# Kernel tuning notes

Measured on AMD Instinct MI355X. Metric: run time of the kernel, lower is better.

The kernel has to match this reference:

```python
import jax, jax.numpy as jnp
import numpy as np

# Cleaned/faithful JAX port of TATLMPLayer. The original torch code has obvious
# typos (edge_type_feature_embedding used before assignment, self.weight_mlp vs
# self._weight_mlp, missing dim= in concatenate, elementwise mult of (B,E,K) with
# (K,D)); we implement the clearly intended math: two-level masked-softmax
# message passing over an incidence matrix H, gumbel-softmax typed edge
# embeddings, and a 4-head cross-attention to polyline features.

NEG_SLOPE = 0.01  # torch leaky_relu default
TAU = 0.5         # gumbel-softmax temperature 1/2


def _mlp(x, W1, b1, W2, b2):
    return jnp.maximum(x @ W1 + b1, 0.0) @ W2 + b2


def setup_inputs() -> dict:
    B, N, E, P, D, T, K, Hd = 2, 256, 512, 256, 128, 8, 8, 256
    key = jax.random.key(0)
    ks = jax.random.split(key, 40)
    g = lambda i, shape, s=0.05: jax.random.normal(ks[i], shape, dtype=jnp.float32) * s
    return {
        "agent_features": jax.random.normal(ks[0], (B, N, D), dtype=jnp.float32),
        "agent_types": jax.random.uniform(ks[1], (B, N, T), dtype=jnp.float32),
        "polyline_features": jax.random.normal(ks[2], (B, P, D), dtype=jnp.float32),
        "H": (jax.random.uniform(ks[3], (B, E, N)) < 0.1).astype(jnp.float32),
        "type_emb": g(4, (K, D)),
        "w_W1": g(5, (2 * D, Hd)), "w_b1": g(6, (Hd,)), "w_W2": g(7, (Hd, 1)), "w_b2": g(8, (1,)),
        "d_W1": g(9, (D + T, Hd)), "d_b1": g(10, (Hd,)), "d_W2": g(11, (Hd, K)), "d_b2": g(12, (K,)),
        "f_W1": g(13, (D + T, Hd)), "f_b1": g(14, (Hd,)), "f_W2": g(15, (Hd, 1)), "f_b2": g(16, (1,)),
        "o_W1": g(17, (4 * D, Hd)), "o_b1": g(18, (Hd,)), "o_W2": g(19, (Hd, D)), "o_b2": g(20, (D,)),
        "q_W": g(21, (3 * D, D)), "q_b": g(22, (D,)),
        "k_W": g(23, (D, D)), "k_b": g(24, (D,)),
        "v_W": g(25, (D, D)), "v_b": g(26, (D,)),
        "iq_W": g(27, (D, D)), "iq_b": g(28, (D,)),
        "ik_W": g(29, (D, D)), "ik_b": g(30, (D,)),
        "iv_W": g(31, (D, D)), "iv_b": g(32, (D,)),
        "op_W": g(33, (D, D)), "op_b": g(34, (D,)),
    }


def reference(agent_features, agent_types, polyline_features, H, type_emb,
              w_W1, w_b1, w_W2, w_b2, d_W1, d_b1, d_W2, d_b2,
              f_W1, f_b1, f_W2, f_b2, o_W1, o_b1, o_W2, o_b2,
              q_W, q_b, k_W, k_b, v_W, v_b,
              iq_W, iq_b, ik_W, ik_b, iv_W, iv_b, op_W, op_b):
    B, N, D = agent_features.shape
    E = H.shape[1]

    # level 1: incidence-aggregated edge features
    ef_init = jnp.einsum('ben,bnd->bed', H, agent_features)            # (B,E,D)
    pair = jnp.concatenate([
        jnp.broadcast_to(ef_init[:, :, None, :], (B, E, N, D)),
        jnp.broadcast_to(agent_features[:, None, :, :], (B, E, N, D))], axis=-1)
    ew = _mlp(pair, w_W1, w_b1, w_W2, w_b2)[..., 0]                    # (B,E,N)
    Hw = jax.nn.softmax(ew * H, axis=2) * H
    edge_features = jnp.einsum('ben,bnd->bed', Hw, agent_features)     # (B,E,D)

    # typed edge embedding via gumbel-softmax over edge types
    edge_type = jnp.einsum('ben,bnt->bet', H, agent_types)             # (B,E,T)
    et = jnp.concatenate([edge_features, edge_type], axis=-1)          # (B,E,D+T)
    logits = _mlp(et, d_W1, d_b1, d_W2, d_b2)                          # (B,E,K)
    u = jax.random.uniform(jax.random.key(42), logits.shape, minval=1e-6, maxval=1.0 - 1e-6)
    gumbel = -jnp.log(-jnp.log(u))
    distribution = jax.nn.softmax((logits + gumbel) / TAU, axis=-1)
    factor = jax.nn.sigmoid(_mlp(et, f_W1, f_b1, f_W2, f_b2))          # (B,E,1)
    edge_type_embedding = jnp.einsum('bek,kd->bed', factor * distribution, type_emb)

    # level 2: masked edge->agent message passing
    pair2 = jnp.concatenate([
        jnp.broadcast_to(edge_type_embedding[:, :, None, :], (B, E, N, D)),
        jnp.broadcast_to(agent_features[:, None, :, :], (B, E, N, D))], axis=-1)
    pair2 = pair2 * H[..., None]
    hw2 = jnp.where(_mlp(pair2, w_W1, w_b1, w_W2, w_b2)[..., 0] > 0,
                    _mlp(pair2, w_W1, w_b1, w_W2, w_b2)[..., 0], 0.0)
    # leaky relu (single-eval form)
    raw2 = _mlp(pair2, w_W1, w_b1, w_W2, w_b2)[..., 0]
    hw2 = jnp.where(raw2 > 0, raw2, NEG_SLOPE * raw2)                  # (B,E,N)
    Hw2 = jax.nn.softmax(hw2, axis=2) * H
    msg = jnp.einsum('ben,bef->bnf', Hw2,
                     jnp.concatenate([edge_features, edge_type_embedding], axis=-1))
    agent_feat = jnp.concatenate([msg, agent_features], axis=-1)       # (B,N,3D)

    # cross-attention to polylines (4 heads)
    Q = agent_feat @ q_W + q_b
    Kp = polyline_features @ k_W + k_b
    Vp = polyline_features @ v_W + v_b
    q2 = Q @ iq_W + iq_b
    k2 = Kp @ ik_W + ik_b
    v2 = Vp @ iv_W + iv_b
    nh, hd = 4, D // 4
    qh = q2.reshape(B, N, nh, hd)
    kh = k2.reshape(B, -1, nh, hd)
    vh = v2.reshape(B, -1, nh, hd)
    att = jax.nn.softmax(jnp.einsum('bqhd,bkhd->bhqk', qh, kh) / jnp.sqrt(jnp.float32(hd)), axis=-1)
    o = jnp.einsum('bhqk,bkhd->bqhd', att, vh).reshape(B, N, D)
    polyline_new = o @ op_W + op_b                                     # (B,N,D)

    agent_new = _mlp(jnp.concatenate([agent_feat, polyline_new], axis=-1),
                     o_W1, o_b1, o_W2, o_b2)                           # (B,N,D)
    return agent_new, polyline_new
```

## Files before the change

### kernel.cpp

```cpp
#include <hip/hip_runtime.h>
#include <math.h>

#define BB 2
#define NN 256
#define EE 512
#define PP 256
#define DD 128
#define TT 8
#define KK 8
#define HDIM 256

#define WS_G      0
#define WS_C0     8192
#define WS_V      8256
#define WS_EDGEF  139328
#define WS_ETE    270400
#define WS_HWT    401472
#define WS_K2     663616
#define WS_V2     729152

#define PB_GUM 16
#define PB_V   272
#define PB_END 528

__device__ inline unsigned rotl32(unsigned x, int d){ return (x<<d)|(x>>(32-d)); }

__device__ inline float bits_to_gumbel(unsigned bits){
  float f = __uint_as_float((bits>>9)|0x3f800000u) - 1.0f;
  const float minv = 1e-6f;
  const float maxv = 1.0f - 1e-6f;
  float u = f*(maxv-minv) + minv;
  u = fmaxf(minv, u);
  return -logf(-logf(u));
}

__device__ __forceinline__ void f4fma(float4& a, float x, const float4& w){
  a.x += x*w.x; a.y += x*w.y; a.z += x*w.z; a.w += x*w.w;
}

__device__ __forceinline__ void block_reduce2_sum(float v[2], float* wred){
  int lane = threadIdx.x & 63, wid = threadIdx.x >> 6;
  #pragma unroll
  for (int s=32;s>0;s>>=1){
    #pragma unroll
    for (int r=0;r<2;r++){ v[r] += __shfl_xor(v[r], s, 64); }
  }
  if (lane==0){
    #pragma unroll
    for (int r=0;r<2;r++) wred[wid*2+r]=v[r];
  }
  __syncthreads();
  #pragma unroll
  for (int r=0;r<2;r++)
    v[r] = (wred[0*2+r]+wred[1*2+r]) + (wred[2*2+r]+wred[3*2+r]);
  __syncthreads();
}

__device__ __forceinline__ void mlp128_lds2(const float (*in)[DD], const float* W, const float* bias,
                                            float (*outl)[DD], float* part, int t){
  int c=(t&31)*4, ks=t>>5;
  float4 a[2];
  #pragma unroll
  for (int r=0;r<2;r++) a[r]=make_float4(0.f,0.f,0.f,0.f);
  #pragma unroll 4
  for (int i=ks*16;i<ks*16+16;i++){
    float4 w = *(const float4*)&W[(size_t)i*DD+c];
    #pragma unroll
    for (int r=0;r<2;r++) f4fma(a[r], in[r][i], w);
  }
  #pragma unroll
  for (int r=0;r<2;r++) *(float4*)&part[(ks*2+r)*DD+c]=a[r];
  __syncthreads();
  int cc=t&127, r=t>>7;
  {
    float s=0.f;
    #pragma unroll
    for (int k2=0;k2<8;k2++) s+=part[(k2*2+r)*DD+cc];
    outl[r][cc]=s+bias[cc];
  }
  __syncthreads();
}

__device__ __forceinline__ void mlp128_glob2(const float (*in)[DD], const float* W, const float* bias,
                                             float* dst, int r0, float* part, int t){
  int c=(t&31)*4, ks=t>>5;
  float4 a[2];
  #pragma unroll
  for (int r=0;r<2;r++) a[r]=make_float4(0.f,0.f,0.f,0.f);
  #pragma unroll 4
  for (int i=ks*16;i<ks*16+16;i++){
    float4 w = *(const float4*)&W[(size_t)i*DD+c];
    #pragma unroll
    for (int r=0;r<2;r++) f4fma(a[r], in[r][i], w);
  }
  #pragma unroll
  for (int r=0;r<2;r++) *(float4*)&part[(ks*2+r)*DD+c]=a[r];
  __syncthreads();
  int cc=t&127, r=t>>7;
  {
    float s=0.f;
    #pragma unroll
    for (int k2=0;k2<8;k2++) s+=part[(k2*2+r)*DD+cc];
    dst[(size_t)(r0+r)*DD+cc]=s+bias[cc];
  }
  __syncthreads();
}

__global__ void prep_kernel(float* g, float* c0, const float* w_b1,
                            const float* w_W2, const float* w_b2,
                            const float* af, const float* wW1, float* Vout,
                            const float* pf,
                            const float* kW, const float* kb, const float* ikW, const float* ikb,
                            const float* vW, const float* vb, const float* ivW, const float* ivb,
                            float* k2, float* v2){
  __shared__ float xs[2][DD];
  __shared__ float part[2048];
  __shared__ float wred[16];
  __shared__ float bufB[2][DD];
  int blk = blockIdx.x;
  int t = threadIdx.x;

  if (blk < PB_GUM){
    int j = blk*256 + t;
    {
      const unsigned k0=0u, k1=42u;
      const unsigned ks2 = k0^k1^0x1BD11BDAu;
      unsigned x0 = (unsigned)j, x1 = (unsigned)j + 4096u;
      const int r0_[4]={13,15,26,6}, r1_[4]={17,29,16,24};
      x0 += k0; x1 += k1;
      #pragma unroll
      for(int i=0;i<4;i++){ x0+=x1; x1=rotl32(x1,r0_[i]); x1^=x0; }
      x0+=k1; x1+=ks2+1u;
      #pragma unroll
      for(int i=0;i<4;i++){ x0+=x1; x1=rotl32(x1,r1_[i]); x1^=x0; }
      x0+=ks2; x1+=k0+2u;
      #pragma unroll
      for(int i=0;i<4;i++){ x0+=x1; x1=rotl32(x1,r0_[i]); x1^=x0; }
      x0+=k0; x1+=k1+3u;
      #pragma unroll
      for(int i=0;i<4;i++){ x0+=x1; x1=rotl32(x1,r1_[i]); x1^=x0; }
      x0+=k1; x1+=ks2+4u;
      #pragma unroll
      for(int i=0;i<4;i++){ x0+=x1; x1=rotl32(x1,r0_[i]); x1^=x0; }
      x0+=ks2; x1+=k0+5u;
      g[j]      = bits_to_gumbel(x0);
      g[j+4096] = bits_to_gumbel(x1);
    }
    if (blk == 0){
      float v4[2];
      v4[0] = fmaxf(w_b1[t],0.f)*w_W2[t]; v4[1]=0.f;
      block_reduce2_sum(v4, wred);
      if (t==0) c0[0] = v4[0] + w_b2[0];
    }
  } else if (blk < PB_V){
    int r0 = (blk - PB_GUM)*2;
    const float* W = wW1 + (size_t)DD*HDIM;
    for (int i=t;i<2*DD;i+=256) xs[i>>7][i&127] = af[(size_t)(r0+(i>>7))*DD + (i&127)];
    __syncthreads();
    int c = (t&63)*4, ks = t>>6;
    float4 acc[2];
    #pragma unroll
    for (int r=0;r<2;r++) acc[r]=make_float4(0.f,0.f,0.f,0.f);
    #pragma unroll 8
    for (int i=ks*32; i<ks*32+32; i++){
      float4 w = *(const float4*)&W[(size_t)i*HDIM + c];
      #pragma unroll
      for (int r=0;r<2;r++) f4fma(acc[r], xs[r][i], w);
    }
    #pragma unroll
    for (int r=0;r<2;r++) *(float4*)&part[(ks*2+r)*HDIM + c] = acc[r];
    __syncthreads();
    #pragma unroll
    for (int r=0;r<2;r++){
      float s = (part[(0*2+r)*HDIM+t] + part[(1*2+r)*HDIM+t])
              + (part[(2*2+r)*HDIM+t] + part[(3*2+r)*HDIM+t]);
      Vout[(size_t)(r0+r)*HDIM + t] = s;
    }
  } else {
    int r0 = (blk - PB_V)*2;
    for (int i=t;i<2*DD;i+=256) xs[i>>7][i&127] = pf[(size_t)(r0+(i>>7))*DD + (i&127)];
    __syncthreads();
    mlp128_lds2 (xs, kW, kb, bufB, part, t);
    mlp128_glob2(bufB, ikW, ikb, k2, r0, part, t);
    mlp128_lds2 (xs, vW, vb, bufB, part, t);
    mlp128_glob2(bufB, ivW, ivb, v2, r0, part, t);
  }
}

__global__ __launch_bounds__(512) void edge_kernel(
                            const float* Hm, const float* af, const float* at,
                            const float* Vm,
                            const float* wW1, const float* wb1, const float* wW2, const float* wb2,
                            const float* dW1, const float* db1, const float* dW2, const float* db2,
                            const float* fW1, const float* fb1, const float* fW2, const float* fb2,
                            const float* type_emb, const float* g, const float* c0p,
                            float* edgef_g, float* ete_g, float* HwT){
  __shared__ float bufA[8192];
  __shared__ float w2s[HDIM*KK];
  __shared__ float w2l[HDIM];
  __shared__ float et4[4][144];
  __shared__ float hd4[4][HDIM];
  __shared__ float redsm[512];
  __shared__ float wred[16];
  __shared__ float mred[4], sinv[4];
  __shared__ float facs[4];
  __shared__ float zz[4][KK];
  __shared__ float pzs[4][KK];
  __shared__ float fdv[4][KK];
  __shared__ int   hcnt[4];
  __shared__ int   hcomp[4*256];

  int e0 = blockIdx.x*4;
  int b  = e0 >> 9;
  int t  = threadIdx.x;
  int lane = t & 63, wid = t >> 6;

  if (t < HDIM) w2l[t] = wW2[t];
  for (int i=t;i<HDIM*KK;i+=512) w2s[i] = dW2[i];

  if (wid < 4){
    int r = wid;
    const float* Hrow = Hm + (size_t)(e0+r)*NN;
    int base = 0;
    #pragma unroll
    for (int c4=0;c4<4;c4++){
      int n2 = c4*64 + lane;
      bool pred = (Hrow[n2] != 0.f);
      unsigned long long mask = __ballot(pred);
      int off = __popcll(mask & ((1ull<<lane)-1ull));
      if (pred) hcomp[r*256+base+off] = n2;
      base += __popcll(mask);
    }
    if (lane==0) hcnt[r] = base;
  }
  __syncthreads();
  {
    int d = t & 127, r = t >> 7;
    int tot = hcnt[r];
    float a = 0.f, a2 = 0.f;
    for (int i=0;i<tot;i++){
      int n2 = hcomp[r*256+i];
      a += af[((size_t)b*NN+n2)*DD + d];
      if (d < TT) a2 += at[((size_t)b*NN+n2)*TT + d];
    }
    et4[r][d] = a;
    if (d < TT) et4[r][DD+d] = a2;
  }
  __syncthreads();
  {
    int c=(t&63)*4, ks=t>>6;
    float4 acc[4];
    #pragma unroll
    for (int r=0;r<4;r++) acc[r]=make_float4(0.f,0.f,0.f,0.f);
    #pragma unroll 4
    for (int i=ks*16; i<ks*16+16; i++){
      float4 w = *(const float4*)&wW1[(size_t)i*HDIM + c];
      #pragma unroll
      for (int r=0;r<4;r++) f4fma(acc[r], et4[r][i], w);
    }
    #pragma unroll
    for (int r=0;r<4;r++) *(float4*)&bufA[(ks*4+r)*HDIM + c] = acc[r];
  }
  __syncthreads();
  {
    int h=t&255, rh=t>>8;
    float bv = wb1[h];
    #pragma unroll
    for (int rr=0;rr<2;rr++){
      int r = 2*rh+rr;
      float s=0.f;
      #pragma unroll
      for (int k=0;k<8;k++) s += bufA[(k*4+r)*HDIM + h];
      hd4[r][h] = s + bv;
    }
  }
  __syncthreads();
  {
    int n = t&255, hh = t>>8;
    const float4* Vrow = (const float4*)(Vm + ((size_t)(b*NN)+n)*HDIM);
    float acc[4]={0.f,0.f,0.f,0.f};
    #pragma unroll 4
    for (int ii=hh*32; ii<hh*32+32; ii++){
      float4 v = Vrow[ii];
      float w0=w2l[4*ii+0], w1=w2l[4*ii+1], wc=w2l[4*ii+2], w3=w2l[4*ii+3];
      #pragma unroll
      for (int r=0;r<4;r++){
        acc[r] += fmaxf(hd4[r][4*ii+0]+v.x,0.f)*w0
                + fmaxf(hd4[r][4*ii+1]+v.y,0.f)*w1
                + fmaxf(hd4[r][4*ii+2]+v.z,0.f)*wc
                + fmaxf(hd4[r][4*ii+3]+v.w,0.f)*w3;
      }
    }
    #pragma unroll
    for (int r=0;r<4;r++) bufA[(hh*4+r)*256 + n] = acc[r];
  }
  __syncthreads();
  {
    int n = t&255, rh = t>>8;
    float b2v = wb2[0];
    #pragma unroll
    for (int rr=0;rr<2;rr++){
      int r = 2*rh+rr;
      float hv = Hm[(size_t)(e0+r)*NN + n];
      float xv = (hv!=0.f) ? (bufA[(0*4+r)*256+n] + bufA[(1*4+r)*256+n] + b2v) : 0.f;
      bufA[2048 + r*256 + n] = xv;
    }
  }
  __syncthreads();
  if (wid < 4){
    int r = wid;
    float v0=bufA[2048+r*256+lane],     v1=bufA[2048+r*256+lane+64],
          v2=bufA[2048+r*256+lane+128], v3=bufA[2048+r*256+lane+192];
    float m = fmaxf(fmaxf(v0,v1), fmaxf(v2,v3));
    #pragma unroll
    for (int s2=32;s2>0;s2>>=1) m = fmaxf(m, __shfl_xor(m, s2, 64));
    float ss = (expf(v0-m)+expf(v1-m)) + (expf(v2-m)+expf(v3-m));
    #pragma unroll
    for (int s2=32;s2>0;s2>>=1) ss += __shfl_xor(ss, s2, 64);
    if (lane==0){ mred[r]=m; sinv[r]=1.f/ss; }
  }
  __syncthreads();
  {
    int n = t&255, rh = t>>8;
    #pragma unroll
    for (int rr=0;rr<2;rr++){
      int r = 2*rh+rr;
      float hv = Hm[(size_t)(e0+r)*NN + n];
      float p = expf(bufA[2048+r*256+n] - mred[r]) * sinv[r];
      bufA[3072 + r*256 + n] = (hv!=0.f) ? p : 0.f;
    }
  }
  __syncthreads();
  {
    int d = t & 127, r = t >> 7;
    int tot = hcnt[r];
    float a = 0.f;
    for (int i=0;i<tot;i++){
      int n2 = hcomp[r*256+i];
      a += bufA[3072 + r*256 + n2] * af[((size_t)b*NN+n2)*DD + d];
    }
    et4[r][d] = a;
    edgef_g[(size_t)(e0+r)*DD + d] = a;
  }
  __syncthreads();
  {
    int half = t>>8, tt = t&255;
    int c=(tt&63)*4, ks=tt>>6;
    const float* W = half ? fW1 : dW1;
    float4 acc[4];
    #pragma unroll
    for (int r=0;r<4;r++) acc[r]=make_float4(0.f,0.f,0.f,0.f);
    #pragma unroll 4
    for (int i=ks*34;i<ks*34+34;i++){
      float4 w = *(const float4*)&W[(size_t)i*HDIM+c];
      #pragma unroll
      for (int r=0;r<4;r++) f4fma(acc[r], et4[r][i], w);
    }
    #pragma unroll
    for (int r=0;r<4;r++) *(float4*)&bufA[half*4096 + (ks*4+r)*HDIM + c] = acc[r];
  }
  __syncthreads();
  {
    int h=t&255, rh=t>>8;
    float bd = db1[h], bf = fb1[h], fw = fW2[h];
    float val[2];
    #pragma unroll
    for (int rr=0;rr<2;rr++){
      int r = 2*rh+rr;
      float sd=0.f, sf=0.f;
      #pragma unroll
      for (int k=0;k<4;k++){ sd += bufA[(k*4+r)*HDIM+h]; sf += bufA[4096+(k*4+r)*HDIM+h]; }
      hd4[r][h] = fmaxf(sd+bd, 0.f);
      val[rr] = fmaxf(sf+bf, 0.f)*fw;
    }
    #pragma unroll
    for (int s2=32;s2>0;s2>>=1){
      val[0] += __shfl_xor(val[0], s2, 64);
      val[1] += __shfl_xor(val[1], s2, 64);
    }
    if (lane==0){ wred[wid*2]=val[0]; wred[wid*2+1]=val[1]; }
  }
  __syncthreads();
  if (t<4){
    int r=t;
    int base = (r>=2)?4:0, off = r&1;
    float s = 0.f;
    #pragma unroll
    for (int w=0;w<4;w++) s += wred[(base+w)*2 + off];
    facs[r] = 1.f/(1.f+expf(-(s+fb2[0])));
  }
  __syncthreads();
  {
    int r_ = t>>7, rem = t&127, k_ = rem&7, j_ = rem>>3;
    float lp = 0.f;
    #pragma unroll 4
    for (int i=0;i<16;i++){
      int h = j_ + 16*i;
      lp += hd4[r_][h]*w2s[h*KK + k_];
    }
    redsm[t] = lp;
  }
  __syncthreads();
  if (t < 32){
    int r = t>>3, k = t&7;
    float s = db2[k] + g[(size_t)(e0+r)*KK + k];
    #pragma unroll
    for (int j=0;j<16;j++) s += redsm[r*128 + j*8 + k];
    zz[r][k] = s*2.0f;
  }
  __syncthreads();
  if (t < 32){
    int r = t>>3, k = t&7;
    float m = zz[r][0];
    #pragma unroll
    for (int k2=1;k2<KK;k2++) m = fmaxf(m, zz[r][k2]);
    pzs[r][k] = expf(zz[r][k]-m);
  }
  __syncthreads();
  if (t < 32){
    int r = t>>3, k = t&7;
    float s = 0.f;
    #pragma unroll
    for (int k2=0;k2<KK;k2++) s += pzs[r][k2];
    fdv[r][k] = facs[r]*pzs[r][k]/s;
  }
  __syncthreads();
  {
    int d = t&127, r = t>>7;
    float a = 0.f;
    #pragma unroll
    for (int k=0;k<KK;k++) a += fdv[r][k]*type_emb[(size_t)k*DD + d];
    et4[r][d] = a;
    ete_g[(size_t)(e0+r)*DD + d] = a;
  }
  __syncthreads();
  {
    int c=(t&63)*4, ks=t>>6;
    float4 acc[4];
    #pragma unroll
    for (int r=0;r<4;r++) acc[r]=make_float4(0.f,0.f,0.f,0.f);
    #pragma unroll 4
    for (int i=ks*16; i<ks*16+16; i++){
      float4 w = *(const float4*)&wW1[(size_t)i*HDIM + c];
      #pragma unroll
      for (int r=0;r<4;r++) f4fma(acc[r], et4[r][i], w);
    }
    #pragma unroll
    for (int r=0;r<4;r++) *(float4*)&bufA[(ks*4+r)*HDIM + c] = acc[r];
  }
  __syncthreads();
  {
    int h=t&255, rh=t>>8;
    float bv = wb1[h];
    #pragma unroll
    for (int rr=0;rr<2;rr++){
      int r = 2*rh+rr;
      float s=0.f;
      #pragma unroll
      for (int k=0;k<8;k++) s += bufA[(k*4+r)*HDIM + h];
      hd4[r][h] = s + bv;
    }
  }
  __syncthreads();
  {
    int n = t&255, hh = t>>8;
    const float4* Vrow = (const float4*)(Vm + ((size_t)(b*NN)+n)*HDIM);
    float acc[4]={0.f,0.f,0.f,0.f};
    #pragma unroll 4
    for (int ii=hh*32; ii<hh*32+32; ii++){
      float4 v = Vrow[ii];
      float w0=w2l[4*ii+0], w1=w2l[4*ii+1], wc=w2l[4*ii+2], w3=w2l[4*ii+3];
      #pragma unroll
      for (int r=0;r<4;r++){
        acc[r] += fmaxf(hd4[r][4*ii+0]+v.x,0.f)*w0
                + fmaxf(hd4[r][4*ii+1]+v.y,0.f)*w1
                + fmaxf(hd4[r][4*ii+2]+v.z,0.f)*wc
                + fmaxf(hd4[r][4*ii+3]+v.w,0.f)*w3;
      }
    }
    #pragma unroll
    for (int r=0;r<4;r++) bufA[(hh*4+r)*256 + n] = acc[r];
  }
  __syncthreads();
  {
    int n = t&255, rh = t>>8;
    float b2v = wb2[0];
    float c0 = c0p[0];
    #pragma unroll
    for (int rr=0;rr<2;rr++){
      int r = 2*rh+rr;
      float hv = Hm[(size_t)(e0+r)*NN + n];
      float raw = (hv!=0.f) ? (bufA[(0*4+r)*256+n] + bufA[(1*4+r)*256+n] + b2v) : c0;
      bufA[2048 + r*256 + n] = raw>0.f ? raw : 0.01f*raw;
    }
  }
  __syncthreads();
  if (wid < 4){
    int r = wid;
    float v0=bufA[2048+r*256+lane],     v1=bufA[2048+r*256+lane+64],
          v2=bufA[2048+r*256+lane+128], v3=bufA[2048+r*256+lane+192];
    float m = fmaxf(fmaxf(v0,v1), fmaxf(v2,v3));
    #pragma unroll
    for (int s2=32;s2>0;s2>>=1) m = fmaxf(m, __shfl_xor(m, s2, 64));
    float ss = (expf(v0-m)+expf(v1-m)) + (expf(v2-m)+expf(v3-m));
    #pragma unroll
    for (int s2=32;s2>0;s2>>=1) ss += __shfl_xor(ss, s2, 64);
    if (lane==0){ mred[r]=m; sinv[r]=1.f/ss; }
  }
  __syncthreads();
  if (t < 256){
    int n = t;
    float o[4];
    #pragma unroll
    for (int r=0;r<4;r++){
      float hv = Hm[(size_t)(e0+r)*NN + n];
      float p = expf(bufA[2048+r*256+n] - mred[r]) * sinv[r];
      o[r] = (hv!=0.f) ? p : 0.f;
    }
    int eb = e0 & 511;
    float4 o4; o4.x=o[0]; o4.y=o[1]; o4.z=o[2]; o4.w=o[3];
    *(float4*)(HwT + ((size_t)(b*NN)+n)*EE + eb) = o4;
  }
}

__global__ void agent_kernel(const float* HwT, const float* edgef, const float* ete,
                             const float* af,
                             const float* qW, const float* qb, const float* iqW, const float* iqb,
                             const float* k2, const float* v2,
                             const float* op_W, const float* op_b,
                             const float* oW1, const float* ob1,
                             const float* oW2, const float* ob2,
                             float* pnew, float* anew){
  __shared__ int   ecomp[EE];
  __shared__ float wcomp[EE];
  __shared__ int   wcnt[4];
  __shared__ float agfl[512];
  __shared__ float part[1024];
  __shared__ float Qs[DD];
  __shared__ float qr[DD];
  __shared__ float att[4][PP+1];
  __shared__ float o_l[DD];
  __shared__ float hid[HDIM];
  int bn = blockIdx.x; int b = bn >> 8; int t = threadIdx.x;
  int lane = t & 63, wid = t >> 6;

  {
    const float* wrow = HwT + (size_t)bn*EE;
    int total = 0;
    #pragma unroll
    for (int p=0;p<2;p++){
      int e = p*256 + t;
      float w = wrow[e];
      bool pred = (w != 0.f);
      unsigned long long mask = __ballot(pred);
      if (lane==0) wcnt[wid] = __popcll(mask);
      int off = __popcll(mask & ((1ull<<lane)-1ull));
      __syncthreads();
      int wb = total;
      for (int ww=0; ww<wid; ww++) wb += wcnt[ww];
      if (pred){ ecomp[wb+off] = e; wcomp[wb+off] = w; }
      total += wcnt[0]+wcnt[1]+wcnt[2]+wcnt[3];
      __syncthreads();
    }
    float acc = 0.f;
    const float* srcbase = (t < DD) ? (edgef + (size_t)b*EE*DD + t)
                                    : (ete   + (size_t)b*EE*DD + (t-DD));
    for (int i=0;i<total;i++){
      acc += wcomp[i] * srcbase[(size_t)ecomp[i]*DD];
    }
    agfl[t] = acc;
    if (t < DD) agfl[2*DD+t] = af[(size_t)bn*DD + t];
  }
  __syncthreads();
  int c=(t&31)*4, ps=t>>5;
  {
    float4 a = make_float4(0.f,0.f,0.f,0.f);
    #pragma unroll 4
    for (int i=ps*48;i<ps*48+48;i++){
      float4 w = *(const float4*)&qW[(size_t)i*DD+c];
      f4fma(a, agfl[i], w);
    }
    *(float4*)&part[ps*DD+c]=a;
  }
  __syncthreads();
  if (t<DD){
    float s=0.f;
    #pragma unroll
    for (int k=0;k<8;k++) s+=part[k*DD+t];
    Qs[t]=s+qb[t];
  }
  __syncthreads();
  {
    float4 a = make_float4(0.f,0.f,0.f,0.f);
    #pragma unroll 4
    for (int i=ps*16;i<ps*16+16;i++){
      float4 w = *(const float4*)&iqW[(size_t)i*DD+c];
      f4fma(a, Qs[i], w);
    }
    *(float4*)&part[ps*DD+c]=a;
  }
  __syncthreads();
  if (t<DD){
    float s=0.f;
    #pragma unroll
    for (int k=0;k<8;k++) s+=part[k*DD+t];
    qr[t]=s+iqb[t];
  }
  __syncthreads();
  const float scale = 0.17677669529663687f;
  const float* krow = k2 + ((size_t)(b*PP) + t)*DD;
  #pragma unroll
  for (int h=0;h<4;h++){
    const float4* k4 = (const float4*)(krow + h*32);
    float s = 0.f;
    #pragma unroll
    for (int jj=0;jj<8;jj++){
      float4 kk = k4[jj];
      s += qr[h*32+jj*4+0]*kk.x + qr[h*32+jj*4+1]*kk.y
         + qr[h*32+jj*4+2]*kk.z + qr[h*32+jj*4+3]*kk.w;
    }
    att[h][t] = s*scale;
  }
  __syncthreads();
  {
    int h = wid;
    float v0 = att[h][lane],     v1 = att[h][lane+64],
          ve = att[h][lane+128], v3 = att[h][lane+192];
    float m = fmaxf(fmaxf(v0,v1), fmaxf(ve,v3));
    #pragma unroll
    for (int s2=32;s2>0;s2>>=1) m = fmaxf(m, __shfl_xor(m, s2, 64));
    float e0 = expf(v0-m), e1 = expf(v1-m), e2 = expf(ve-m), e3 = expf(v3-m);
    float ss = (e0+e1)+(e2+e3);
    #pragma unroll
    for (int s2=32;s2>0;s2>>=1) ss += __shfl_xor(ss, s2, 64);
    float inv = 1.f/ss;
    att[h][lane] = e0*inv; att[h][lane+64] = e1*inv;
    att[h][lane+128] = e2*inv; att[h][lane+192] = e3*inv;
  }
  __syncthreads();
  int h2 = c >> 5;
  {
    float4 acc = make_float4(0.f,0.f,0.f,0.f);
    #pragma unroll 4
    for (int i=0;i<32;i++){
      int p = ps*32+i;
      float4 v = *(const float4*)&v2[((size_t)(b*PP)+p)*DD + c];
      f4fma(acc, att[h2][p], v);
    }
    *(float4*)&part[ps*DD+c]=acc;
  }
  __syncthreads();
  if (t<DD){
    float s=0.f;
    #pragma unroll
    for (int k=0;k<8;k++) s+=part[k*DD+t];
    o_l[t]=s;
  }
  __syncthreads();
  {
    float4 a2 = make_float4(0.f,0.f,0.f,0.f);
    #pragma unroll 4
    for (int i=ps*16;i<ps*16+16;i++){
      float4 w = *(const float4*)&op_W[(size_t)i*DD + c];
      f4fma(a2, o_l[i], w);
    }
    *(float4*)&part[ps*DD+c]=a2;
  }
  __syncthreads();
  if (t<DD){
    float s=0.f;
    #pragma unroll
    for (int k=0;k<8;k++) s+=part[k*DD+t];
    float pv = s+op_b[t];
    agfl[3*DD+t] = pv;
    pnew[(size_t)bn*DD+t] = pv;
  }
  __syncthreads();
  {
    int c1=(t&63)*4, ks1=t>>6;
    float4 acc = make_float4(0.f,0.f,0.f,0.f);
    #pragma unroll 8
    for (int i=ks1*128;i<ks1*128+128;i++){
      float4 w = *(const float4*)&oW1[(size_t)i*HDIM+c1];
      f4fma(acc, agfl[i], w);
    }
    *(float4*)&part[ks1*HDIM+c1]=acc;
  }
  __syncthreads();
  {
    float s = (part[0*HDIM+t]+part[1*HDIM+t]) + (part[2*HDIM+t]+part[3*HDIM+t]);
    hid[t] = fmaxf(s+ob1[t], 0.f);
  }
  __syncthreads();
  {
    float4 a2 = make_float4(0.f,0.f,0.f,0.f);
    #pragma unroll 8
    for (int h=ps*32;h<ps*32+32;h++){
      float4 w = *(const float4*)&oW2[(size_t)h*DD+c];
      f4fma(a2, hid[h], w);
    }
    *(float4*)&part[ps*DD+c]=a2;
  }
  __syncthreads();
  if (t<DD){
    float s=0.f;
    #pragma unroll
    for (int k=0;k<8;k++) s+=part[k*DD+t];
    anew[(size_t)bn*DD+t]=s+ob2[t];
  }
}

extern "C" void kernel_launch(void* const* d_in, const int* in_sizes, int n_in,
                              void* d_out, int out_size, void* d_ws, size_t ws_size,
                              hipStream_t stream) {
  const float* af       = (const float*)d_in[0];
  const float* at       = (const float*)d_in[1];
  const float* pf       = (const float*)d_in[2];
  const float* Hm       = (const float*)d_in[3];
  const float* type_emb = (const float*)d_in[4];
  const float* w_W1 = (const float*)d_in[5];
  const float* w_b1 = (const float*)d_in[6];
  const float* w_W2 = (const float*)d_in[7];
  const float* w_b2 = (const float*)d_in[8];
  const float* d_W1 = (const float*)d_in[9];
  const float* d_b1 = (const float*)d_in[10];
  const float* d_W2 = (const float*)d_in[11];
  const float* d_b2 = (const float*)d_in[12];
  const float* f_W1 = (const float*)d_in[13];
  const float* f_b1 = (const float*)d_in[14];
  const float* f_W2 = (const float*)d_in[15];
  const float* f_b2 = (const float*)d_in[16];
  const float* o_W1 = (const float*)d_in[17];
  const float* o_b1 = (const float*)d_in[18];
  const float* o_W2 = (const float*)d_in[19];
  const float* o_b2 = (const float*)d_in[20];
  const float* q_W  = (const float*)d_in[21];
  const float* q_b  = (const float*)d_in[22];
  const float* k_W  = (const float*)d_in[23];
  const float* k_b  = (const float*)d_in[24];
  const float* v_W  = (const float*)d_in[25];
  const float* v_b  = (const float*)d_in[26];
  const float* iq_W = (const float*)d_in[27];
  const float* iq_b = (const float*)d_in[28];
  const float* ik_W = (const float*)d_in[29];
  const float* ik_b = (const float*)d_in[30];
  const float* iv_W = (const float*)d_in[31];
  const float* iv_b = (const float*)d_in[32];
  const float* op_W = (const float*)d_in[33];
  const float* op_b = (const float*)d_in[34];

  float* ws   = (float*)d_ws;
  float* out  = (float*)d_out;
  float* anew = out;
  float* pnew = out + BB*NN*DD;

  prep_kernel<<<PB_END, 256, 0, stream>>>(
      ws+WS_G, ws+WS_C0, w_b1, w_W2, w_b2,
      af, w_W1, ws+WS_V,
      pf, k_W,k_b,ik_W,ik_b, v_W,v_b,iv_W,iv_b,
      ws+WS_K2, ws+WS_V2);
  edge_kernel<<<256,512,0,stream>>>(
      Hm, af, at, ws+WS_V,
      w_W1, w_b1, w_W2, w_b2,
      d_W1,d_b1,d_W2,d_b2, f_W1,f_b1,f_W2,f_b2,
      type_emb, ws+WS_G, ws+WS_C0,
      ws+WS_EDGEF, ws+WS_ETE, ws+WS_HWT);
  agent_kernel<<<BB*NN,256,0,stream>>>(
      ws+WS_HWT, ws+WS_EDGEF, ws+WS_ETE, af,
      q_W, q_b, iq_W, iq_b,
      ws+WS_K2, ws+WS_V2, op_W, op_b,
      o_W1,o_b1,o_W2,o_b2, pnew, anew);
}
```

Before: 90.60 us.

## Move edge first-layer precompute into prep kernel and process two agents per block

The incidence gather and first MLP layer for edges (edge-sum features, type sums, hidden layer U1) move from the edge kernel into extra blocks of the prep kernel, so that work runs in parallel with the other prep blocks. The edge kernel now preloads its w_W1 slice into registers for the later second-level matmul. The agent kernel handles two agents per 512-thread block, so each weight load serves two rows. This adds workspace traffic and register pressure (16 float4 per thread in the edge kernel), which could lower occupancy.

```diff
diff --git a/kernel.cpp b/kernel.cpp
--- a/kernel.cpp
+++ b/kernel.cpp
@@ -13,15 +13,18 @@
 #define WS_G      0
 #define WS_C0     8192
 #define WS_V      8256
-#define WS_EDGEF  139328
-#define WS_ETE    270400
-#define WS_HWT    401472
-#define WS_K2     663616
-#define WS_V2     729152
+#define WS_U1     139328
+#define WS_ETYPE  401472
+#define WS_EDGEF  409664
+#define WS_ETE    540736
+#define WS_HWT    671808
+#define WS_K2     933952
+#define WS_V2     999488
 
 #define PB_GUM 16
-#define PB_V   272
-#define PB_END 528
+#define PB_INC 272
+#define PB_V   528
+#define PB_END 784
 
 __device__ inline unsigned rotl32(unsigned x, int d){ return (x<<d)|(x>>(32-d)); }
 
@@ -108,17 +111,23 @@
 
 __global__ void prep_kernel(float* g, float* c0, const float* w_b1,
                             const float* w_W2, const float* w_b2,
-                            const float* af, const float* wW1, float* Vout,
+                            const float* Hm, const float* af, const float* at,
+                            const float* wW1, const float* wb1,
+                            float* U1g, float* etype_g, float* Vout,
                             const float* pf,
                             const float* kW, const float* kb, const float* ikW, const float* ikb,
                             const float* vW, const float* vb, const float* ivW, const float* ivb,
                             float* k2, float* v2){
+  __shared__ float part[4096];
+  __shared__ float wred[16];
+  __shared__ int   hcomp[4*256];
+  __shared__ int   hcnt[4];
+  __shared__ float ef[4][DD];
   __shared__ float xs[2][DD];
-  __shared__ float part[2048];
-  __shared__ float wred[16];
   __shared__ float bufB[2][DD];
   int blk = blockIdx.x;
   int t = threadIdx.x;
+  int lane = t & 63, wid = t >> 6;
 
   if (blk < PB_GUM){
     int j = blk*256 + t;
@@ -152,8 +161,68 @@
       block_reduce2_sum(v4, wred);
       if (t==0) c0[0] = v4[0] + w_b2[0];
     }
+  } else if (blk < PB_INC){
+    int e0 = (blk - PB_GUM)*4;
+    int b = e0 >> 9;
+    {
+      int r = wid;
+      const float* Hrow = Hm + (size_t)(e0+r)*NN;
+      int base = 0;
+      #pragma unroll
+      for (int c4=0;c4<4;c4++){
+        int n2 = c4*64 + lane;
+        bool pred = (Hrow[n2] != 0.f);
+        unsigned long long mask = __ballot(pred);
+        int off = __popcll(mask & ((1ull<<lane)-1ull));
+        if (pred) hcomp[r*256+base+off] = n2;
+        base += __popcll(mask);
+      }
+      if (lane==0) hcnt[r] = base;
+    }
+    __syncthreads();
+    {
+      int d = t & 127, eh = t >> 7;
+      #pragma unroll
+      for (int rr=0;rr<2;rr++){
+        int r = eh*2 + rr;
+        int tot = hcnt[r];
+        float a = 0.f, a2 = 0.f;
+        for (int i=0;i<tot;i++){
+          int n2 = hcomp[r*256+i];
+          a += af[((size_t)b*NN+n2)*DD + d];
+          if (d < TT) a2 += at[((size_t)b*NN+n2)*TT + d];
+        }
+        ef[r][d] = a;
+        if (d < TT) etype_g[(size_t)(e0+r)*TT + d] = a2;
+      }
+    }
+    __syncthreads();
+    {
+      int c = (t&63)*4, ks = t>>6;
+      float4 acc[4];
+      #pragma unroll
+      for (int r=0;r<4;r++) acc[r]=make_float4(0.f,0.f,0.f,0.f);
+      #pragma unroll 8
+      for (int i=ks*32; i<ks*32+32; i++){
+        float4 w = *(const float4*)&wW1[(size_t)i*HDIM + c];
+        #pragma unroll
+        for (int r=0;r<4;r++) f4fma(acc[r], ef[r][i], w);
+      }
+      #pragma unroll
+      for (int r=0;r<4;r++) *(float4*)&part[(ks*4+r)*HDIM + c] = acc[r];
+    }
+    __syncthreads();
+    {
+      float bv = wb1[t];
+      #pragma unroll
+      for (int r=0;r<4;r++){
+        float s = (part[(0*4+r)*HDIM+t] + part[(1*4+r)*HDIM+t])
+                + (part[(2*4+r)*HDIM+t] + part[(3*4+r)*HDIM+t]);
+        U1g[(size_t)(e0+r)*HDIM + t] = s + bv;
+      }
+    }
   } else if (blk < PB_V){
-    int r0 = (blk - PB_GUM)*2;
+    int r0 = (blk - PB_INC)*2;
     const float* W = wW1 + (size_t)DD*HDIM;
     for (int i=t;i<2*DD;i+=256) xs[i>>7][i&127] = af[(size_t)(r0+(i>>7))*DD + (i&127)];
     __syncthreads();
@@ -188,8 +257,8 @@
 }
 
 __global__ __launch_bounds__(512) void edge_kernel(
-                            const float* Hm, const float* af, const float* at,
-                            const float* Vm,
+                            const float* Hm, const float* af,
+                            const float* Vm, const float* U1g, const float* etype_g,
                             const float* wW1, const float* wb1, const float* wW2, const float* wb2,
                             const float* dW1, const float* db1, const float* dW2, const float* db2,
                             const float* fW1, const float* fb1, const float* fW2, const float* fb2,
@@ -215,9 +284,23 @@
   int t  = threadIdx.x;
   int lane = t & 63, wid = t >> 6;
 
+  int cW=(t&63)*4, ksW=t>>6;
+  float4 wreg[16];
+  #pragma unroll
+  for (int i=0;i<16;i++)
+    wreg[i] = *(const float4*)&wW1[(size_t)(ksW*16+i)*HDIM + cW];
+
   if (t < HDIM) w2l[t] = wW2[t];
   for (int i=t;i<HDIM*KK;i+=512) w2s[i] = dW2[i];
-
+  {
+    int h=t&255, rh=t>>8;
+    #pragma unroll
+    for (int rr=0;rr<2;rr++){
+      int r = 2*rh+rr;
+      hd4[r][h] = U1g[(size_t)(e0+r)*HDIM + h];
+    }
+  }
+  if (t < 32){ int r=t>>3, j=t&7; et4[r][DD+j] = etype_g[(size_t)(e0+r)*TT + j]; }
   if (wid < 4){
     int r = wid;
     const float* Hrow = Hm + (size_t)(e0+r)*NN;
@@ -235,47 +318,6 @@
   }
   __syncthreads();
   {
-    int d = t & 127, r = t >> 7;
-    int tot = hcnt[r];
-    float a = 0.f, a2 = 0.f;
-    for (int i=0;i<tot;i++){
-      int n2 = hcomp[r*256+i];
-      a += af[((size_t)b*NN+n2)*DD + d];
-      if (d < TT) a2 += at[((size_t)b*NN+n2)*TT + d];
-    }
-    et4[r][d] = a;
-    if (d < TT) et4[r][DD+d] = a2;
-  }
-  __syncthreads();
-  {
-    int c=(t&63)*4, ks=t>>6;
-    float4 acc[4];
-    #pragma unroll
-    for (int r=0;r<4;r++) acc[r]=make_float4(0.f,0.f,0.f,0.f);
-    #pragma unroll 4
-    for (int i=ks*16; i<ks*16+16; i++){
-      float4 w = *(const float4*)&wW1[(size_t)i*HDIM + c];
-      #pragma unroll
-      for (int r=0;r<4;r++) f4fma(acc[r], et4[r][i], w);
-    }
-    #pragma unroll
-    for (int r=0;r<4;r++) *(float4*)&bufA[(ks*4+r)*HDIM + c] = acc[r];
-  }
-  __syncthreads();
-  {
-    int h=t&255, rh=t>>8;
-    float bv = wb1[h];
-    #pragma unroll
-    for (int rr=0;rr<2;rr++){
-      int r = 2*rh+rr;
-      float s=0.f;
-      #pragma unroll
-      for (int k=0;k<8;k++) s += bufA[(k*4+r)*HDIM + h];
-      hd4[r][h] = s + bv;
-    }
-  }
-  __syncthreads();
-  {
     int n = t&255, hh = t>>8;
     const float4* Vrow = (const float4*)(Vm + ((size_t)(b*NN)+n)*HDIM);
     float acc[4]={0.f,0.f,0.f,0.f};
@@ -435,18 +477,17 @@
   }
   __syncthreads();
   {
-    int c=(t&63)*4, ks=t>>6;
     float4 acc[4];
     #pragma unroll
     for (int r=0;r<4;r++) acc[r]=make_float4(0.f,0.f,0.f,0.f);
-    #pragma unroll 4
-    for (int i=ks*16; i<ks*16+16; i++){
-      float4 w = *(const float4*)&wW1[(size_t)i*HDIM + c];
-      #pragma unroll
-      for (int r=0;r<4;r++) f4fma(acc[r], et4[r][i], w);
-    }
-    #pragma unroll
-    for (int r=0;r<4;r++) *(float4*)&bufA[(ks*4+r)*HDIM + c] = acc[r];
+    #pragma unroll
+    for (int i=0;i<16;i++){
+      int idx = ksW*16 + i;
+      #pragma unroll
+      for (int r=0;r<4;r++) f4fma(acc[r], et4[r][idx], wreg[i]);
+    }
+    #pragma unroll
+    for (int r=0;r<4;r++) *(float4*)&bufA[(ksW*4+r)*HDIM + cW] = acc[r];
   }
   __syncthreads();
   {
@@ -523,7 +564,8 @@
   }
 }
 
-__global__ void agent_kernel(const float* HwT, const float* edgef, const float* ete,
+__global__ __launch_bounds__(512) void agent_kernel(
+                             const float* HwT, const float* edgef, const float* ete,
                              const float* af,
                              const float* qW, const float* qb, const float* iqW, const float* iqb,
                              const float* k2, const float* v2,
@@ -531,63 +573,67 @@
                              const float* oW1, const float* ob1,
                              const float* oW2, const float* ob2,
                              float* pnew, float* anew){
-  __shared__ int   ecomp[EE];
-  __shared__ float wcomp[EE];
-  __shared__ int   wcnt[4];
-  __shared__ float agfl[512];
-  __shared__ float part[1024];
-  __shared__ float Qs[DD];
-  __shared__ float qr[DD];
-  __shared__ float att[4][PP+1];
-  __shared__ float o_l[DD];
-  __shared__ float hid[HDIM];
-  int bn = blockIdx.x; int b = bn >> 8; int t = threadIdx.x;
+  __shared__ int   ecomp[2][EE];
+  __shared__ float wcomp[2][EE];
+  __shared__ int   wcnt[2][4];
+  __shared__ float agfl[2][512];
+  __shared__ float part[4096];
+  __shared__ float Qs[2][DD];
+  __shared__ float qr[2][DD];
+  __shared__ float att[2][4][PP+1];
+  __shared__ float o_l[2][DD];
+  __shared__ float hid[2][HDIM];
+  int n0 = blockIdx.x*2; int b = n0 >> 8; int t = threadIdx.x;
+  int tt = t & 255, rr = t >> 8;
   int lane = t & 63, wid = t >> 6;
-
-  {
+  int lw = tt >> 6;
+
+  {
+    int bn = n0 + rr;
     const float* wrow = HwT + (size_t)bn*EE;
     int total = 0;
     #pragma unroll
     for (int p=0;p<2;p++){
-      int e = p*256 + t;
+      int e = p*256 + tt;
       float w = wrow[e];
       bool pred = (w != 0.f);
       unsigned long long mask = __ballot(pred);
-      if (lane==0) wcnt[wid] = __popcll(mask);
+      if (lane==0) wcnt[rr][lw] = __popcll(mask);
       int off = __popcll(mask & ((1ull<<lane)-1ull));
       __syncthreads();
       int wb = total;
-      for (int ww=0; ww<wid; ww++) wb += wcnt[ww];
-      if (pred){ ecomp[wb+off] = e; wcomp[wb+off] = w; }
-      total += wcnt[0]+wcnt[1]+wcnt[2]+wcnt[3];
+      for (int ww=0; ww<lw; ww++) wb += wcnt[rr][ww];
+      if (pred){ ecomp[rr][wb+off] = e; wcomp[rr][wb+off] = w; }
+      total += wcnt[rr][0]+wcnt[rr][1]+wcnt[rr][2]+wcnt[rr][3];
       __syncthreads();
     }
     float acc = 0.f;
-    const float* srcbase = (t < DD) ? (edgef + (size_t)b*EE*DD + t)
-                                    : (ete   + (size_t)b*EE*DD + (t-DD));
+    const float* srcbase = (tt < DD) ? (edgef + (size_t)b*EE*DD + tt)
+                                     : (ete   + (size_t)b*EE*DD + (tt-DD));
     for (int i=0;i<total;i++){
-      acc += wcomp[i] * srcbase[(size_t)ecomp[i]*DD];
-    }
-    agfl[t] = acc;
-    if (t < DD) agfl[2*DD+t] = af[(size_t)bn*DD + t];
-  }
-  __syncthreads();
-  int c=(t&31)*4, ps=t>>5;
+      acc += wcomp[rr][i] * srcbase[(size_t)ecomp[rr][i]*DD];
+    }
+    agfl[rr][tt] = acc;
+    if (tt < DD) agfl[rr][2*DD+tt] = af[(size_t)bn*DD + tt];
+  }
+  __syncthreads();
+  int c=(tt&31)*4, ps=tt>>5;
   {
     float4 a = make_float4(0.f,0.f,0.f,0.f);
     #pragma unroll 4
     for (int i=ps*48;i<ps*48+48;i++){
       float4 w = *(const float4*)&qW[(size_t)i*DD+c];
-      f4fma(a, agfl[i], w);
-    }
-    *(float4*)&part[ps*DD+c]=a;
-  }
-  __syncthreads();
-  if (t<DD){
+      f4fma(a, agfl[rr][i], w);
+    }
+    *(float4*)&part[(rr*8+ps)*DD+c]=a;
+  }
+  __syncthreads();
+  if (t<256){
+    int cc=t&127, r=t>>7;
     float s=0.f;
     #pragma unroll
-    for (int k=0;k<8;k++) s+=part[k*DD+t];
-    Qs[t]=s+qb[t];
+    for (int k=0;k<8;k++) s+=part[(r*8+k)*DD+cc];
+    Qs[r][cc]=s+qb[cc];
   }
   __syncthreads();
   {
@@ -595,37 +641,44 @@
     #pragma unroll 4
     for (int i=ps*16;i<ps*16+16;i++){
       float4 w = *(const float4*)&iqW[(size_t)i*DD+c];
-      f4fma(a, Qs[i], w);
-    }
-    *(float4*)&part[ps*DD+c]=a;
-  }
-  __syncthreads();
-  if (t<DD){
+      f4fma(a, Qs[rr][i], w);
+    }
+    *(float4*)&part[(rr*8+ps)*DD+c]=a;
+  }
+  __syncthreads();
+  if (t<256){
+    int cc=t&127, r=t>>7;
     float s=0.f;
     #pragma unroll
-    for (int k=0;k<8;k++) s+=part[k*DD+t];
-    qr[t]=s+iqb[t];
+    for (int k=0;k<8;k++) s+=part[(r*8+k)*DD+cc];
+    qr[r][cc]=s+iqb[cc];
   }
   __syncthreads();
   const float scale = 0.17677669529663687f;
-  const float* krow = k2 + ((size_t)(b*PP) + t)*DD;
-  #pragma unroll
-  for (int h=0;h<4;h++){
-    const float4* k4 = (const float4*)(krow + h*32);
-    float s = 0.f;
-    #pragma unroll
-    for (int jj=0;jj<8;jj++){
-      float4 kk = k4[jj];
-      s += qr[h*32+jj*4+0]*kk.x + qr[h*32+jj*4+1]*kk.y
-         + qr[h*32+jj*4+2]*kk.z + qr[h*32+jj*4+3]*kk.w;
-    }
-    att[h][t] = s*scale;
-  }
-  __syncthreads();
-  {
-    int h = wid;
-    float v0 = att[h][lane],     v1 = att[h][lane+64],
-          ve = att[h][lane+128], v3 = att[h][lane+192];
+  {
+    const float* krow = k2 + ((size_t)(b*PP) + tt)*DD;
+    #pragma unroll
+    for (int hh=0;hh<2;hh++){
+      int h = rr*2+hh;
+      const float4* k4 = (const float4*)(krow + h*32);
+      float s0=0.f, s1=0.f;
+      #pragma unroll
+      for (int jj=0;jj<8;jj++){
+        float4 kk = k4[jj];
+        s0 += qr[0][h*32+jj*4+0]*kk.x + qr[0][h*32+jj*4+1]*kk.y
+            + qr[0][h*32+jj*4+2]*kk.z + qr[0][h*32+jj*4+3]*kk.w;
+        s1 += qr[1][h*32+jj*4+0]*kk.x + qr[1][h*32+jj*4+1]*kk.y
+            + qr[1][h*32+jj*4+2]*kk.z + qr[1][h*32+jj*4+3]*kk.w;
+      }
+      att[0][h][tt] = s0*scale;
+      att[1][h][tt] = s1*scale;
+    }
+  }
+  __syncthreads();
+  {
+    int r = wid>>2, h = wid&3;
+    float v0 = att[r][h][lane],     v1 = att[r][h][lane+64],
+          ve = att[r][h][lane+128], v3 = att[r][h][lane+192];
     float m = fmaxf(fmaxf(v0,v1), fmaxf(ve,v3));
     #pragma unroll
     for (int s2=32;s2>0;s2>>=1) m = fmaxf(m, __shfl_xor(m, s2, 64));
@@ -634,8 +687,8 @@
     #pragma unroll
     for (int s2=32;s2>0;s2>>=1) ss += __shfl_xor(ss, s2, 64);
     float inv = 1.f/ss;
-    att[h][lane] = e0*inv; att[h][lane+64] = e1*inv;
-    att[h][lane+128] = e2*inv; att[h][lane+192] = e3*inv;
+    att[r][h][lane] = e0*inv; att[r][h][lane+64] = e1*inv;
+    att[r][h][lane+128] = e2*inv; att[r][h][lane+192] = e3*inv;
   }
   __syncthreads();
   int h2 = c >> 5;
@@ -645,16 +698,17 @@
     for (int i=0;i<32;i++){
       int p = ps*32+i;
       float4 v = *(const float4*)&v2[((size_t)(b*PP)+p)*DD + c];
-      f4fma(acc, att[h2][p], v);
-    }
-    *(float4*)&part[ps*DD+c]=acc;
-  }
-  __syncthreads();
-  if (t<DD){
+      f4fma(acc, att[rr][h2][p], v);
+    }
+    *(float4*)&part[(rr*8+ps)*DD+c]=acc;
+  }
+  __syncthreads();
+  if (t<256){
+    int cc=t&127, r=t>>7;
     float s=0.f;
     #pragma unroll
-    for (int k=0;k<8;k++) s+=part[k*DD+t];
-    o_l[t]=s;
+    for (int k=0;k<8;k++) s+=part[(r*8+k)*DD+cc];
+    o_l[r][cc]=s;
   }
   __syncthreads();
   {
@@ -662,34 +716,42 @@
     #pragma unroll 4
     for (int i=ps*16;i<ps*16+16;i++){
       float4 w = *(const float4*)&op_W[(size_t)i*DD + c];
-      f4fma(a2, o_l[i], w);
-    }
-    *(float4*)&part[ps*DD+c]=a2;
-  }
-  __syncthreads();
-  if (t<DD){
+      f4fma(a2, o_l[rr][i], w);
+    }
+    *(float4*)&part[(rr*8+ps)*DD+c]=a2;
+  }
+  __syncthreads();
+  if (t<256){
+    int cc=t&127, r=t>>7;
     float s=0.f;
     #pragma unroll
-    for (int k=0;k<8;k++) s+=part[k*DD+t];
-    float pv = s+op_b[t];
-    agfl[3*DD+t] = pv;
-    pnew[(size_t)bn*DD+t] = pv;
+    for (int k=0;k<8;k++) s+=part[(r*8+k)*DD+cc];
+    float pv = s+op_b[cc];
+    agfl[r][3*DD+cc] = pv;
+    pnew[(size_t)(n0+r)*DD+cc] = pv;
   }
   __syncthreads();
   {
     int c1=(t&63)*4, ks1=t>>6;
-    float4 acc = make_float4(0.f,0.f,0.f,0.f);
+    float4 acc[2];
+    #pragma unroll
+    for (int r=0;r<2;r++) acc[r]=make_float4(0.f,0.f,0.f,0.f);
     #pragma unroll 8
-    for (int i=ks1*128;i<ks1*128+128;i++){
+    for (int i=ks1*64;i<ks1*64+64;i++){
       float4 w = *(const float4*)&oW1[(size_t)i*HDIM+c1];
-      f4fma(acc, agfl[i], w);
-    }
-    *(float4*)&part[ks1*HDIM+c1]=acc;
-  }
-  __syncthreads();
-  {
-    float s = (part[0*HDIM+t]+part[1*HDIM+t]) + (part[2*HDIM+t]+part[3*HDIM+t]);
-    hid[t] = fmaxf(s+ob1[t], 0.f);
+      f4fma(acc[0], agfl[0][i], w);
+      f4fma(acc[1], agfl[1][i], w);
+    }
+    #pragma unroll
+    for (int r=0;r<2;r++) *(float4*)&part[(ks1*2+r)*HDIM+c1]=acc[r];
+  }
+  __syncthreads();
+  {
+    int h=t&255, r=t>>8;
+    float s=0.f;
+    #pragma unroll
+    for (int k=0;k<8;k++) s+=part[(k*2+r)*HDIM+h];
+    hid[r][h] = fmaxf(s+ob1[h], 0.f);
   }
   __syncthreads();
   {
@@ -697,16 +759,17 @@
     #pragma unroll 8
     for (int h=ps*32;h<ps*32+32;h++){
       float4 w = *(const float4*)&oW2[(size_t)h*DD+c];
-      f4fma(a2, hid[h], w);
-    }
-    *(float4*)&part[ps*DD+c]=a2;
-  }
-  __syncthreads();
-  if (t<DD){
+      f4fma(a2, hid[rr][h], w);
+    }
+    *(float4*)&part[(rr*8+ps)*DD+c]=a2;
+  }
+  __syncthreads();
+  if (t<256){
+    int cc=t&127, r=t>>7;
     float s=0.f;
     #pragma unroll
-    for (int k=0;k<8;k++) s+=part[k*DD+t];
-    anew[(size_t)bn*DD+t]=s+ob2[t];
+    for (int k=0;k<8;k++) s+=part[(r*8+k)*DD+cc];
+    anew[(size_t)(n0+r)*DD+cc]=s+ob2[cc];
   }
 }
 
@@ -756,16 +819,17 @@
 
   prep_kernel<<<PB_END, 256, 0, stream>>>(
       ws+WS_G, ws+WS_C0, w_b1, w_W2, w_b2,
-      af, w_W1, ws+WS_V,
+      Hm, af, at, w_W1, w_b1,
+      ws+WS_U1, ws+WS_ETYPE, ws+WS_V,
       pf, k_W,k_b,ik_W,ik_b, v_W,v_b,iv_W,iv_b,
       ws+WS_K2, ws+WS_V2);
   edge_kernel<<<256,512,0,stream>>>(
-      Hm, af, at, ws+WS_V,
+      Hm, af, ws+WS_V, ws+WS_U1, ws+WS_ETYPE,
       w_W1, w_b1, w_W2, w_b2,
       d_W1,d_b1,d_W2,d_b2, f_W1,f_b1,f_W2,f_b2,
       type_emb, ws+WS_G, ws+WS_C0,
       ws+WS_EDGEF, ws+WS_ETE, ws+WS_HWT);
-  agent_kernel<<<BB*NN,256,0,stream>>>(
+  agent_kernel<<<256,512,0,stream>>>(
       ws+WS_HWT, ws+WS_EDGEF, ws+WS_ETE, af,
       q_W, q_b, iq_W, iq_b,
       ws+WS_K2, ws+WS_V2, op_W, op_b,
```

After: 89.44 us. Within noise of the previous version (-1.3%).
